# Optimization experiments

Hardware: AMD Instinct MI355X
Metric: run time of the kernel (lower is better)

The kernel has to match this reference:

```python
import jax, jax.numpy as jnp
import numpy as np

HID = 400
K = 10  # attention mixture components


def _lstm_cell(x, h, c, Wih, Whh, b):
    # torch gate order: i, f, g, o
    g = x @ Wih.T + h @ Whh.T + b
    i, f, gg, o = jnp.split(g, 4, axis=-1)
    c = jax.nn.sigmoid(f) * c + jax.nn.sigmoid(i) * jnp.tanh(gg)
    h = jax.nn.sigmoid(o) * jnp.tanh(c)
    return h, c


def setup_inputs() -> dict:
    key = jax.random.key(0)
    ks = jax.random.split(key, 14)
    B, T, U, D = 64, 600, 64, 60
    s = 0.08  # keep exp() in attention numerically tame
    strokes = jax.random.normal(ks[0], (B, T, 3), dtype=jnp.float32)
    ids = jax.random.randint(ks[1], (B, U), 0, D)
    onehots = jax.nn.one_hot(ids, D, dtype=jnp.float32)
    text_mask = jnp.ones((B, U), dtype=jnp.float32)
    W_ih1 = jax.random.normal(ks[2], (4 * HID, D + 3)) * s
    W_hh1 = jax.random.normal(ks[3], (4 * HID, HID)) * s
    b1 = jax.random.normal(ks[4], (4 * HID,)) * s  # b_ih + b_hh combined
    W_win = jax.random.normal(ks[5], (3 * K, HID)) * s
    b_win = jax.random.normal(ks[6], (3 * K,)) * s
    W_ih2 = jax.random.normal(ks[7], (4 * HID, 3 + D + HID)) * s
    W_hh2 = jax.random.normal(ks[8], (4 * HID, HID)) * s
    b2 = jax.random.normal(ks[9], (4 * HID,)) * s
    W_fc = jax.random.normal(ks[10], (121, 2 * HID)) * s
    b_fc = jax.random.normal(ks[11], (121,)) * s
    return {"strokes": strokes, "onehots": onehots, "text_mask": text_mask,
            "W_ih1": W_ih1, "W_hh1": W_hh1, "b1": b1,
            "W_win": W_win, "b_win": b_win,
            "W_ih2": W_ih2, "W_hh2": W_hh2, "b2": b2,
            "W_fc": W_fc, "b_fc": b_fc}


def reference(strokes, onehots, text_mask, W_ih1, W_hh1, b1, W_win, b_win,
              W_ih2, W_hh2, b2, W_fc, b_fc):
    B, T, _ = strokes.shape
    U = onehots.shape[1]
    u = jnp.arange(U, dtype=jnp.float32)

    def step1(carry, x_t):
        h0, c0, kappa, w = carry
        h0, c0 = _lstm_cell(jnp.concatenate([x_t, w], -1), h0, c0, W_ih1, W_hh1, b1)
        p = jnp.exp(h0 @ W_win.T + b_win)              # [B, 3K]
        alpha, beta, kap = jnp.split(p, 3, axis=-1)    # each [B, K]
        kappa = kappa + kap
        diff = kappa[:, None, :] - u[None, :, None]    # [B, U, K]
        phi = jnp.sum(alpha[:, None, :] * jnp.exp(-beta[:, None, :] * diff * diff), -1)
        phi = phi * text_mask                          # [B, U]
        w = jnp.einsum('bu,bud->bd', phi, onehots)     # [B, D]
        return (h0, c0, kappa, w), (h0, w, phi)

    z = jnp.zeros((B, HID), jnp.float32)
    init = (z, z, jnp.zeros((B, K), jnp.float32), onehots[:, 0, :])
    (h0f, c0f, kappa_f, w_f), (H1, Wt, Phi) = jax.lax.scan(step1, init, strokes.transpose(1, 0, 2))
    lstm1_out = H1.transpose(1, 0, 2)                  # [B, T, 400]
    attn_out = Wt.transpose(1, 0, 2)                   # [B, T, D]
    phi_last = Phi[-1]

    x2 = jnp.concatenate([strokes, attn_out, lstm1_out], -1)  # [B, T, 463]

    def step2(carry, x_t):
        h, c = carry
        h, c = _lstm_cell(x_t, h, c, W_ih2, W_hh2, b2)
        return (h, c), h

    (h1f, c1f), H2 = jax.lax.scan(step2, (z, z), x2.transpose(1, 0, 2))
    lstm2_out = H2.transpose(1, 0, 2)                  # [B, T, 400]

    out = jnp.concatenate([lstm1_out, lstm2_out], -1) @ W_fc.T + b_fc  # [B, T, 121]
    mu, log_sigma, pi, rho, eos = jnp.split(out, [40, 80, 100, 120], axis=-1)
    rho = jnp.tanh(rho)
    pi = jax.nn.softmax(pi, axis=-1)
    eos = jax.nn.sigmoid(-eos)
    mu = mu.reshape(B, T, 20, 2)
    sigma = log_sigma.reshape(B, T, 20, 2)  # original returns raw log-sigma reshaped
    return (pi, mu, sigma, rho, eos, w_f, kappa_f, phi_last, h0f, c0f, h1f, c1f)
```

## Files before the change

### kernel.cpp

```cpp
#include <hip/hip_runtime.h>
#include <hip/hip_bf16.h>
#include <math.h>

#define HIDN 400
#define KK   10
#define UU   64
#define DD   60
#define TT   600
#define FCIN 800
#define FCOUT 121

#define NH1  100
#define NH2  100
#define NWBK 32
#define WBAT 2
#define TOTB 232
#define THR  1024
#define NWAVE 16
#define CB   16
#define PSTR 68

#define SLOT1 25600
#define SLOTW 3840

#define PI_OFF    0
#define MU_OFF    768000
#define SIG_OFF   2304000
#define RHO_OFF   3840000
#define EOS_OFF   4608000
#define WF_OFF    4646400
#define KAPPA_OFF 4650240
#define PHI_OFF   4650880
#define H0F_OFF   4654976
#define C0F_OFF   4680576
#define H1F_OFF   4706176
#define C1F_OFF   4731776

#define WS_H1T   0
#define WS_H2T   15385600
#define WS_WHT   30771200
#define WS_XST   33079040
#define WS_WALL1 33194240
#define WS_WALL2 33935040
#define WS_WFCT  35315840
#define WS_CNT   35412640

#define CAI(i,g) ((((i)&7)*13+(g))*16)
#define CWI(i,g) (1664 + (((i)&7)*4+(g))*16)
#define CHI(i,g) (2176 + (((i)&7)*13+(g))*16)
#define CNT_INTS 3840

#define SMEM_F 32512

__device__ __forceinline__ float sigm(float x){ return 1.0f/(1.0f + expf(-x)); }
__device__ __forceinline__ int tgtn(int i, int n){ return n*((i>>3)+1); }

__device__ __forceinline__ void st_agent(float* p, float v){
  __hip_atomic_store(p, v, __ATOMIC_RELAXED, __HIP_MEMORY_SCOPE_AGENT);
}
__device__ __forceinline__ int ld_agent_i(const int* p){
  return __hip_atomic_load(p, __ATOMIC_RELAXED, __HIP_MEMORY_SCOPE_AGENT);
}
__device__ __forceinline__ void arrive(int* p){
  __hip_atomic_fetch_add(p, 1, __ATOMIC_RELAXED, __HIP_MEMORY_SCOPE_AGENT);
}
__device__ __forceinline__ void spin_ge(const int* w, int tgt){
  if (ld_agent_i(w) >= tgt) return;
  do { __builtin_amdgcn_s_sleep(1); } while (ld_agent_i(w) < tgt);
}

__global__ void prep_init(const float* __restrict__ onehots, const float* __restrict__ strokes,
                          float* __restrict__ H1t, float* __restrict__ H2t,
                          float* __restrict__ Wh,  float* __restrict__ XST,
                          int* __restrict__ cnts){
  int idx = blockIdx.x*blockDim.x + threadIdx.x;
  if (idx < SLOT1){ H1t[idx] = 0.f; H2t[idx] = 0.f; }
  if (idx < SLOTW){
    int d = idx >> 6, b = idx & 63;
    Wh[idx] = onehots[b*(UU*DD) + d];
  }
  if (idx < TT*3*64){
    int t = idx/192, rem = idx%192, comp = rem/64, b = rem%64;
    XST[idx] = strokes[(b*TT + t)*3 + comp];
  }
  if (idx < CNT_INTS) cnts[idx] = 0;
}

__global__ void prep_wall(const float* __restrict__ Wih1, const float* __restrict__ Whh1,
                          const float* __restrict__ Wih2, const float* __restrict__ Whh2,
                          float* __restrict__ WALL1, float* __restrict__ WALL2){
  int idx = blockIdx.x*blockDim.x + threadIdx.x;
  if (idx < 640000){
    int g = idx/400, k = idx%400;
    int q = g/400, j = g%400, pp = j>>2, c = 4*q + (j&3);
    WALL1[((size_t)pp*463 + k)*CB + c] = Whh1[idx];
  } else if (idx < 740800){
    int s = idx - 640000;
    int g = s/63, col = s%63;
    int q = g/400, j = g%400, pp = j>>2, c = 4*q + (j&3);
    int r = (col < 3) ? (460 + col) : (400 + col - 3);
    WALL1[((size_t)pp*463 + r)*CB + c] = Wih1[s];
  } else if (idx < 1380800){
    int s = idx - 740800;
    int g = s/400, k = s%400;
    int q = g/400, j = g%400, pp = j>>2, c = 4*q + (j&3);
    WALL2[((size_t)pp*863 + 400 + k)*CB + c] = Whh2[s];
  } else if (idx < 2121600){
    int s = idx - 1380800;
    int g = s/463, col = s%463;
    int q = g/400, j = g%400, pp = j>>2, c = 4*q + (j&3);
    int r = (col<3) ? (860+col) : (col<63 ? (800+col-3) : (col-63));
    WALL2[((size_t)pp*863 + r)*CB + c] = Wih2[s];
  }
}

__global__ void prep_wfc(const float* __restrict__ Wfc, float* __restrict__ WfcT){
  int idx = blockIdx.x*blockDim.x + threadIdx.x;
  if (idx >= FCIN*FCOUT) return;
  int k = idx / FCOUT, j = idx - k*FCOUT;
  WfcT[idx] = Wfc[j*FCIN + k];
}

__device__ __forceinline__ void gemv16(const float* __restrict__ x,
                                       const float* __restrict__ w,
                                       int n, int bg4, int cg4, float acc[16]){
  #pragma unroll 4
  for (int k=0;k<n;++k){
    const float4 xv = *(const float4*)(x + k*64 + bg4);
    const float4 wv = *(const float4*)(w + k*CB + cg4);
    acc[0]  = fmaf(wv.x, xv.x, acc[0]);
    acc[1]  = fmaf(wv.x, xv.y, acc[1]);
    acc[2]  = fmaf(wv.x, xv.z, acc[2]);
    acc[3]  = fmaf(wv.x, xv.w, acc[3]);
    acc[4]  = fmaf(wv.y, xv.x, acc[4]);
    acc[5]  = fmaf(wv.y, xv.y, acc[5]);
    acc[6]  = fmaf(wv.y, xv.z, acc[6]);
    acc[7]  = fmaf(wv.y, xv.w, acc[7]);
    acc[8]  = fmaf(wv.z, xv.x, acc[8]);
    acc[9]  = fmaf(wv.z, xv.y, acc[9]);
    acc[10] = fmaf(wv.z, xv.z, acc[10]);
    acc[11] = fmaf(wv.z, xv.w, acc[11]);
    acc[12] = fmaf(wv.w, xv.x, acc[12]);
    acc[13] = fmaf(wv.w, xv.y, acc[13]);
    acc[14] = fmaf(wv.w, xv.z, acc[14]);
    acc[15] = fmaf(wv.w, xv.w, acc[15]);
  }
}

__global__ __launch_bounds__(THR) void recurrent_kernel(
    const float* __restrict__ Wwin, const float* __restrict__ bwin,
    const float* __restrict__ b1g,  const float* __restrict__ b2g,
    const float* __restrict__ tmask,const float* __restrict__ onehots,
    const float* __restrict__ WALL1,const float* __restrict__ WALL2,
    float* __restrict__ H1t,        float* __restrict__ H2t,
    float* __restrict__ Wh,         const float* __restrict__ XST,
    int* __restrict__ cnts,         float* __restrict__ outp)
{
  const int p   = blockIdx.x;
  const int tid = threadIdx.x;
  __shared__ float SM[SMEM_F];

  if (p < NH1){
    const int wave = tid >> 6, lane = tid & 63;
    const int bg4  = (lane & 15) * 4;
    const int cg4  = (lane >> 4) * 4;
    float* WL1 = SM;          float* PART = SM + 7408;
    float* GRED= SM + 24816;  float* CS   = SM + 25840;
    float* BS  = SM + 26096;

    for (int idx = tid; idx < 463*CB; idx += THR) WL1[idx] = WALL1[(size_t)p*463*CB + idx];
    if (tid < 16){ int q = tid>>2, u = tid&3; BS[tid] = b1g[q*HIDN + 4*p + u]; }
    if (tid < 256) CS[tid] = 0.f;
    __syncthreads();

    for (int i = 0; i < TT; ++i){
      if (i >= 1){
        if (tid < 13) spin_ge(&cnts[CAI(i-1, tid)], tgtn(i-1, tid==12?4:8));
        asm volatile("" ::: "memory");
        __syncthreads();
      }
      float acc[16];
      #pragma unroll
      for (int z=0; z<16; ++z) acc[z] = 0.f;
      {
        const float* __restrict__ H1prev = H1t + (size_t)i*SLOT1;
        int k0 = wave*26, k1 = min(k0 + 26, 403);
        { int ka = k0, kb = min(k1, 400);
          if (kb > ka) gemv16(H1prev + ka*64, WL1 + ka*CB, kb-ka, bg4, cg4, acc); }
        { int ka = max(k0,400), kb = k1;
          if (kb > ka) gemv16(XST + i*192 + (ka-400)*64, WL1 + (460+(ka-400))*CB, kb-ka, bg4, cg4, acc); }
      }
      #pragma unroll
      for (int cc=0; cc<4; ++cc)
        *(float4*)&PART[(wave*16 + cg4 + cc)*PSTR + bg4] =
          make_float4(acc[cc*4+0], acc[cc*4+1], acc[cc*4+2], acc[cc*4+3]);
      __syncthreads();
      {
        int c = tid>>6, b = tid&63; float s = 0.f;
        #pragma unroll
        for (int w16=0; w16<NWAVE; ++w16) s += PART[(w16*16 + c)*PSTR + b];
        GRED[c*64 + b] = s;
      }
      __syncthreads();
      if (i >= 1){
        if (tid < 4) spin_ge(&cnts[CWI(i-1, tid)], tgtn(i-1, 8));
        asm volatile("" ::: "memory");
        __syncthreads();
      }
      if (tid < 256){
        int u = tid>>6, b = tid&63, j = 4*p + u;
        float gi = GRED[( 0+u)*64+b] + BS[ 0+u];
        float gf = GRED[( 4+u)*64+b] + BS[ 4+u];
        float gg = GRED[( 8+u)*64+b] + BS[ 8+u];
        float go = GRED[(12+u)*64+b] + BS[12+u];
        const float* __restrict__ Whp = Wh + (size_t)i*SLOTW + b;
        const float* __restrict__ Ww  = WL1 + 400*CB + u;
        #pragma unroll 4
        for (int d = 0; d < DD; ++d){
          float wv = Whp[d*64];
          gi = fmaf(wv, Ww[d*CB     ], gi);
          gf = fmaf(wv, Ww[d*CB +  4], gf);
          gg = fmaf(wv, Ww[d*CB +  8], gg);
          go = fmaf(wv, Ww[d*CB + 12], go);
        }
        float c_ = sigm(gf)*CS[u*64+b] + sigm(gi)*tanhf(gg);
        float h_ = sigm(go)*tanhf(c_);
        CS[u*64+b] = c_;
        st_agent(&H1t[(size_t)(i+1)*SLOT1 + j*64 + b], h_);
        if (i == TT-1){ outp[H0F_OFF + b*HIDN + j] = h_; outp[C0F_OFF + b*HIDN + j] = c_; }
      }
      __syncthreads();
      if (tid == 0) arrive(&cnts[CAI(i, p>>3)]);
    }
  } else if (p < NH1 + NH2){
    const int q2 = p - NH1;
    const int wave = tid >> 6, lane = tid & 63;
    const int bg4  = (lane & 15) * 4;
    const int cg4  = (lane >> 4) * 4;
    float* WL2 = SM;          float* PART = SM + 13808;
    float* GRED= SM + 31216;  float* CS   = SM + 32240;
    float* BS  = SM + 32496;

    for (int idx = tid; idx < 863*CB; idx += THR) WL2[idx] = WALL2[(size_t)q2*863*CB + idx];
    if (tid < 16){ int q = tid>>2, u = tid&3; BS[tid] = b2g[q*HIDN + 4*q2 + u]; }
    if (tid < 256) CS[tid] = 0.f;
    __syncthreads();

    for (int t2 = 0; t2 < TT; ++t2){
      if (tid < 13) spin_ge(&cnts[CAI(t2, tid)], tgtn(t2, tid==12?4:8));
      else if (tid >= 64 && tid < 68) spin_ge(&cnts[CWI(t2, tid-64)], tgtn(t2, 8));
      asm volatile("" ::: "memory");
      __syncthreads();
      float acc[16];
      #pragma unroll
      for (int z=0; z<16; ++z) acc[z] = 0.f;
      {
        const float* __restrict__ H1v = H1t + (size_t)(t2+1)*SLOT1;
        const float* __restrict__ Whv = Wh  + (size_t)(t2+1)*SLOTW;
        int k0 = wave*29, k1 = min(k0 + 29, 463);
        { int ka = k0, kb = min(k1, 400);
          if (kb > ka) gemv16(H1v + ka*64, WL2 + ka*CB, kb-ka, bg4, cg4, acc); }
        { int ka = max(k0,400), kb = min(k1, 460);
          if (kb > ka) gemv16(Whv + (ka-400)*64, WL2 + (800+(ka-400))*CB, kb-ka, bg4, cg4, acc); }
        { int ka = max(k0,460), kb = k1;
          if (kb > ka) gemv16(XST + t2*192 + (ka-460)*64, WL2 + (860+(ka-460))*CB, kb-ka, bg4, cg4, acc); }
      }
      if (t2 >= 1){
        if (tid < 13) spin_ge(&cnts[CHI(t2-1, tid)], tgtn(t2-1, tid==12?4:8));
        asm volatile("" ::: "memory");
        __syncthreads();
      }
      {
        const float* __restrict__ H2v = H2t + (size_t)t2*SLOT1;
        int k0 = wave*25, k1 = min(k0 + 25, 400);
        if (k1 > k0) gemv16(H2v + k0*64, WL2 + (400+k0)*CB, k1-k0, bg4, cg4, acc);
      }
      #pragma unroll
      for (int cc=0; cc<4; ++cc)
        *(float4*)&PART[(wave*16 + cg4 + cc)*PSTR + bg4] =
          make_float4(acc[cc*4+0], acc[cc*4+1], acc[cc*4+2], acc[cc*4+3]);
      __syncthreads();
      {
        int c = tid>>6, b = tid&63; float s = 0.f;
        #pragma unroll
        for (int w16=0; w16<NWAVE; ++w16) s += PART[(w16*16 + c)*PSTR + b];
        GRED[c*64 + b] = s;
      }
      __syncthreads();
      if (tid < 256){
        int u = tid>>6, b = tid&63, j = 4*q2 + u;
        float gi = GRED[( 0+u)*64+b] + BS[ 0+u];
        float gf = GRED[( 4+u)*64+b] + BS[ 4+u];
        float gg = GRED[( 8+u)*64+b] + BS[ 8+u];
        float go = GRED[(12+u)*64+b] + BS[12+u];
        float c_ = sigm(gf)*CS[u*64+b] + sigm(gi)*tanhf(gg);
        float h_ = sigm(go)*tanhf(c_);
        CS[u*64+b] = c_;
        st_agent(&H2t[(size_t)(t2+1)*SLOT1 + j*64 + b], h_);
        if (t2 == TT-1){ outp[H1F_OFF + b*HIDN + j] = h_; outp[C1F_OFF + b*HIDN + j] = c_; }
      }
      __syncthreads();
      if (tid == 0) arrive(&cnts[CHI(t2, q2>>3)]);
    }
  } else {
    const int wb = p - NH1 - NH2;
    const int b0 = wb * WBAT;
    float* WWT = SM;          float* ONE = SM + 13200;
    float* H1S = SM + 20880;  float* TMS = SM + 22080;
    float* PW  = SM + 22208;  float* KAP = SM + 22272;
    float* PHI = SM + 22304;

    for (int idx = tid; idx < 30*400; idx += THR){
      int j = idx/400, k = idx - j*400;
      WWT[k*33 + j] = Wwin[idx];
    }
    for (int idx = tid; idx < WBAT*UU*DD; idx += THR) ONE[idx] = onehots[b0*(UU*DD) + idx];
    if (tid < WBAT*UU) TMS[tid] = tmask[b0*UU + tid];
    if (tid < WBAT*16) KAP[tid] = 0.f;
    __syncthreads();

    for (int i = 0; i < TT; ++i){
      if (tid < 13) spin_ge(&cnts[CAI(i, tid)], tgtn(i, tid==12?4:8));
      asm volatile("" ::: "memory");
      __syncthreads();
      const float* __restrict__ H1now = H1t + (size_t)(i+1)*SLOT1;
      if (tid < 400){
        float2 v = *(const float2*)&H1now[tid*64 + b0];
        H1S[tid*3 + 0] = v.x;
        H1S[tid*3 + 1] = v.y;
      }
      __syncthreads();
      if (tid < 960){
        int ks = tid & 15, pair = tid >> 4;
        int b = pair / 30, j = pair - b*30;
        float s = 0.f;
        #pragma unroll
        for (int kk = 0; kk < 25; ++kk){
          int k = ks*25 + kk;
          s = fmaf(H1S[k*3 + b], WWT[k*33 + j], s);
        }
        s += __shfl_down(s, 8, 16);
        s += __shfl_down(s, 4, 16);
        s += __shfl_down(s, 2, 16);
        s += __shfl_down(s, 1, 16);
        if (ks == 0) PW[b*32 + j] = expf(s + bwin[j]);
      }
      __syncthreads();
      if (tid < WBAT*KK){
        int b = tid/KK, k = tid - b*KK;
        KAP[b*16 + k] += PW[b*32 + 20 + k];
      }
      __syncthreads();
      if (tid < WBAT*UU){
        int b = tid >> 6, u = tid & 63;
        float uf = (float)u, s = 0.f;
        #pragma unroll
        for (int q = 0; q < KK; ++q){
          float d = KAP[b*16 + q] - uf;
          s = fmaf(PW[b*32 + q], expf(-PW[b*32 + 10 + q]*d*d), s);
        }
        s *= TMS[b*64 + u];
        PHI[b*64 + u] = s;
        if (i == TT-1) outp[PHI_OFF + (b0+b)*UU + u] = s;
      }
      __syncthreads();
      if (tid < WBAT*DD){
        int b = tid/DD, d = tid - b*DD;
        float s = 0.f;
        #pragma unroll 8
        for (int u = 0; u < UU; ++u) s = fmaf(PHI[b*64 + u], ONE[b*(UU*DD) + u*DD + d], s);
        st_agent(&Wh[(size_t)(i+1)*SLOTW + d*64 + b0 + b], s);
        if (i == TT-1) outp[WF_OFF + (b0+b)*DD + d] = s;
      }
      if (i == TT-1 && tid < WBAT*KK){
        int b = tid/KK, k = tid - b*KK;
        outp[KAPPA_OFF + (b0+b)*KK + k] = KAP[b*16 + k];
      }
      __syncthreads();
      if (tid == 0) arrive(&cnts[CWI(i, wb>>3)]);
    }
  }
}

__global__ __launch_bounds__(128) void fc2_kernel(
    const float* __restrict__ H1t, const float* __restrict__ H2t,
    const float* __restrict__ WfcT, const float* __restrict__ bfc,
    float* __restrict__ outp)
{
  const int t   = blockIdx.x;
  const int tid = threadIdx.x;
  __shared__ float Xs[8][64];
  __shared__ float OUT[FCOUT][65];
  float acc[64];
  #pragma unroll
  for (int b=0;b<64;++b) acc[b]=0.f;
  const float* __restrict__ base1 = H1t + (size_t)(t+1)*SLOT1;
  const float* __restrict__ base2 = H2t + (size_t)(t+1)*SLOT1;

  for (int kb=0; kb<100; ++kb){
    __syncthreads();
    #pragma unroll
    for (int e=0;e<4;++e){
      int idx = e*128 + tid;
      int row = idx>>6, b = idx&63;
      int k = kb*8 + row;
      Xs[row][b] = (k<400) ? base1[k*64+b] : base2[(k-400)*64+b];
    }
    __syncthreads();
    if (tid < FCOUT){
      #pragma unroll
      for (int kk=0;kk<8;++kk){
        float wv = WfcT[(kb*8+kk)*FCOUT + tid];
        #pragma unroll
        for (int b4=0;b4<16;++b4){
          float4 xv = *(const float4*)&Xs[kk][b4*4];
          acc[b4*4+0] = fmaf(wv, xv.x, acc[b4*4+0]);
          acc[b4*4+1] = fmaf(wv, xv.y, acc[b4*4+1]);
          acc[b4*4+2] = fmaf(wv, xv.z, acc[b4*4+2]);
          acc[b4*4+3] = fmaf(wv, xv.w, acc[b4*4+3]);
        }
      }
    }
  }
  if (tid < FCOUT){
    float bj = bfc[tid];
    #pragma unroll
    for (int b=0;b<64;++b) OUT[tid][b] = acc[b] + bj;
  }
  __syncthreads();
  if (tid < 64){
    const int b = tid;
    const size_t pos = (size_t)b*TT + t;
    for (int j=0;j<40;++j) outp[MU_OFF  + pos*40 + j] = OUT[j][b];
    for (int j=0;j<40;++j) outp[SIG_OFF + pos*40 + j] = OUT[40+j][b];
    float m = -1e30f;
    for (int q=0;q<20;++q) m = fmaxf(m, OUT[80+q][b]);
    float e[20], s=0.f;
    for (int q=0;q<20;++q){ e[q]=expf(OUT[80+q][b]-m); s+=e[q]; }
    float inv = 1.f/s;
    for (int q=0;q<20;++q) outp[PI_OFF  + pos*20 + q] = e[q]*inv;
    for (int q=0;q<20;++q) outp[RHO_OFF + pos*20 + q] = tanhf(OUT[100+q][b]);
    outp[EOS_OFF + pos] = 1.0f/(1.0f + expf(OUT[120][b]));
  }
}

extern "C" void kernel_launch(void* const* d_in, const int* in_sizes, int n_in,
                              void* d_out, int out_size, void* d_ws, size_t ws_size,
                              hipStream_t stream){
  (void)in_sizes; (void)n_in; (void)out_size; (void)ws_size;
  const float* strokes = (const float*)d_in[0];
  const float* onehots = (const float*)d_in[1];
  const float* tmask   = (const float*)d_in[2];
  const float* Wih1    = (const float*)d_in[3];
  const float* Whh1    = (const float*)d_in[4];
  const float* b1      = (const float*)d_in[5];
  const float* Wwin    = (const float*)d_in[6];
  const float* bwin    = (const float*)d_in[7];
  const float* Wih2    = (const float*)d_in[8];
  const float* Whh2    = (const float*)d_in[9];
  const float* b2      = (const float*)d_in[10];
  const float* Wfc     = (const float*)d_in[11];
  const float* bfc     = (const float*)d_in[12];

  float* ws    = (float*)d_ws;
  float* outp  = (float*)d_out;
  float* H1t   = ws + WS_H1T;
  float* H2t   = ws + WS_H2T;
  float* Wh    = ws + WS_WHT;
  float* XST   = ws + WS_XST;
  float* WALL1 = ws + WS_WALL1;
  float* WALL2 = ws + WS_WALL2;
  float* WfcT  = ws + WS_WFCT;
  int*   cnts  = (int*)(ws + WS_CNT);

  hipLaunchKernelGGL(prep_init, dim3((TT*3*64 + 255)/256), dim3(256), 0, stream,
                     onehots, strokes, H1t, H2t, Wh, XST, cnts);
  hipLaunchKernelGGL(prep_wall, dim3((2121600 + 255)/256), dim3(256), 0, stream,
                     Wih1, Whh1, Wih2, Whh2, WALL1, WALL2);
  hipLaunchKernelGGL(prep_wfc, dim3((FCIN*FCOUT + 255)/256), dim3(256), 0, stream,
                     Wfc, WfcT);

  hipLaunchKernelGGL(recurrent_kernel, dim3(TOTB), dim3(THR), 0, stream,
                     Wwin, bwin, b1, b2, tmask, onehots, WALL1, WALL2,
                     H1t, H2t, Wh, XST, cnts, outp);

  hipLaunchKernelGGL(fc2_kernel, dim3(TT), dim3(128), 0, stream,
                     H1t, H2t, WfcT, bfc, outp);
}
```

Before: 6.567 ms.

## Split LSTM1 batch into two interleaved halves to overlap with attention blocks

The layer-1 recurrent blocks now process the 64-sample batch as two 32-sample groups in alternating half-steps, each with its own per-group counters. Attention blocks are split by group and wait only on their own half. While one half waits on its attention result, the other half's GEMV can proceed, which is meant to hide the serial dependency chain between LSTM1 and the attention window. The cost is twice as many barriers and spin-waits per timestep, plus narrower GEMV tiles.

```diff
diff --git a/kernel.cpp b/kernel.cpp
--- a/kernel.cpp
+++ b/kernel.cpp
@@ -19,6 +19,7 @@
 #define NWAVE 16
 #define CB   16
 #define PSTR 68
+#define PSTR2 36
 
 #define SLOT1 25600
 #define SLOTW 3840
@@ -45,10 +46,10 @@
 #define WS_WFCT  35315840
 #define WS_CNT   35412640
 
-#define CAI(i,g) ((((i)&7)*13+(g))*16)
-#define CWI(i,g) (1664 + (((i)&7)*4+(g))*16)
-#define CHI(i,g) (2176 + (((i)&7)*13+(g))*16)
-#define CNT_INTS 3840
+#define CAI(grp,i,g) ((((grp)*8 + ((i)&7))*13 + (g))*16)
+#define CWI(grp,i,g) (3328 + (((grp)*8 + ((i)&7))*2 + (g))*16)
+#define CHI(i,g)     (3840 + (((i)&7)*13 + (g))*16)
+#define CNT_INTS 5504
 
 #define SMEM_F 32512
 
@@ -146,6 +147,23 @@
     acc[15] = fmaf(wv.w, xv.w, acc[15]);
   }
 }
+__device__ __forceinline__ void gemv8(const float* __restrict__ x,
+                                      const float* __restrict__ w,
+                                      int n, int bg4, int cg2, float acc[8]){
+  #pragma unroll 4
+  for (int k=0;k<n;++k){
+    const float4 xv = *(const float4*)(x + k*64 + bg4);
+    const float2 wv = *(const float2*)(w + k*CB + cg2);
+    acc[0] = fmaf(wv.x, xv.x, acc[0]);
+    acc[1] = fmaf(wv.x, xv.y, acc[1]);
+    acc[2] = fmaf(wv.x, xv.z, acc[2]);
+    acc[3] = fmaf(wv.x, xv.w, acc[3]);
+    acc[4] = fmaf(wv.y, xv.x, acc[4]);
+    acc[5] = fmaf(wv.y, xv.y, acc[5]);
+    acc[6] = fmaf(wv.y, xv.z, acc[6]);
+    acc[7] = fmaf(wv.y, xv.w, acc[7]);
+  }
+}
 
 __global__ __launch_bounds__(THR) void recurrent_kernel(
     const float* __restrict__ Wwin, const float* __restrict__ bwin,
@@ -162,58 +180,56 @@
 
   if (p < NH1){
     const int wave = tid >> 6, lane = tid & 63;
-    const int bg4  = (lane & 15) * 4;
-    const int cg4  = (lane >> 4) * 4;
+    const int bg4  = (lane & 7) * 4;
+    const int cg2  = (lane >> 3) * 2;
     float* WL1 = SM;          float* PART = SM + 7408;
-    float* GRED= SM + 24816;  float* CS   = SM + 25840;
-    float* BS  = SM + 26096;
+    float* GRED= SM + 16624;  float* CS   = SM + 17136;
+    float* BS  = SM + 17392;
 
     for (int idx = tid; idx < 463*CB; idx += THR) WL1[idx] = WALL1[(size_t)p*463*CB + idx];
     if (tid < 16){ int q = tid>>2, u = tid&3; BS[tid] = b1g[q*HIDN + 4*p + u]; }
     if (tid < 256) CS[tid] = 0.f;
     __syncthreads();
 
-    for (int i = 0; i < TT; ++i){
+    for (int j = 0; j < 2*TT; ++j){
+      const int grp = j & 1, i = j >> 1;
+      const int gb  = grp * 32;
       if (i >= 1){
-        if (tid < 13) spin_ge(&cnts[CAI(i-1, tid)], tgtn(i-1, tid==12?4:8));
+        if (tid < 13) spin_ge(&cnts[CAI(grp, i-1, tid)], tgtn(i-1, tid==12?4:8));
         asm volatile("" ::: "memory");
         __syncthreads();
       }
-      float acc[16];
-      #pragma unroll
-      for (int z=0; z<16; ++z) acc[z] = 0.f;
+      float acc[8] = {0,0,0,0,0,0,0,0};
       {
-        const float* __restrict__ H1prev = H1t + (size_t)i*SLOT1;
+        const float* __restrict__ H1prev = H1t + (size_t)i*SLOT1 + gb;
         int k0 = wave*26, k1 = min(k0 + 26, 403);
         { int ka = k0, kb = min(k1, 400);
-          if (kb > ka) gemv16(H1prev + ka*64, WL1 + ka*CB, kb-ka, bg4, cg4, acc); }
+          if (kb > ka) gemv8(H1prev + ka*64, WL1 + ka*CB, kb-ka, bg4, cg2, acc); }
         { int ka = max(k0,400), kb = k1;
-          if (kb > ka) gemv16(XST + i*192 + (ka-400)*64, WL1 + (460+(ka-400))*CB, kb-ka, bg4, cg4, acc); }
-      }
-      #pragma unroll
-      for (int cc=0; cc<4; ++cc)
-        *(float4*)&PART[(wave*16 + cg4 + cc)*PSTR + bg4] =
-          make_float4(acc[cc*4+0], acc[cc*4+1], acc[cc*4+2], acc[cc*4+3]);
-      __syncthreads();
-      {
-        int c = tid>>6, b = tid&63; float s = 0.f;
+          if (kb > ka) gemv8(XST + i*192 + (ka-400)*64 + gb, WL1 + (460+(ka-400))*CB, kb-ka, bg4, cg2, acc); }
+      }
+      *(float4*)&PART[(wave*16 + cg2  )*PSTR2 + bg4] = make_float4(acc[0],acc[1],acc[2],acc[3]);
+      *(float4*)&PART[(wave*16 + cg2+1)*PSTR2 + bg4] = make_float4(acc[4],acc[5],acc[6],acc[7]);
+      __syncthreads();
+      if (tid < 512){
+        int c = tid>>5, b = tid&31; float s = 0.f;
         #pragma unroll
-        for (int w16=0; w16<NWAVE; ++w16) s += PART[(w16*16 + c)*PSTR + b];
-        GRED[c*64 + b] = s;
+        for (int w16=0; w16<NWAVE; ++w16) s += PART[(w16*16 + c)*PSTR2 + b];
+        GRED[c*32 + b] = s;
       }
       __syncthreads();
       if (i >= 1){
-        if (tid < 4) spin_ge(&cnts[CWI(i-1, tid)], tgtn(i-1, 8));
+        if (tid < 2) spin_ge(&cnts[CWI(grp, i-1, tid)], tgtn(i-1, 8));
         asm volatile("" ::: "memory");
         __syncthreads();
       }
-      if (tid < 256){
-        int u = tid>>6, b = tid&63, j = 4*p + u;
-        float gi = GRED[( 0+u)*64+b] + BS[ 0+u];
-        float gf = GRED[( 4+u)*64+b] + BS[ 4+u];
-        float gg = GRED[( 8+u)*64+b] + BS[ 8+u];
-        float go = GRED[(12+u)*64+b] + BS[12+u];
-        const float* __restrict__ Whp = Wh + (size_t)i*SLOTW + b;
+      if (tid < 128){
+        int u = tid>>5, b = tid&31, jj = 4*p + u;
+        float gi = GRED[( 0+u)*32+b] + BS[ 0+u];
+        float gf = GRED[( 4+u)*32+b] + BS[ 4+u];
+        float gg = GRED[( 8+u)*32+b] + BS[ 8+u];
+        float go = GRED[(12+u)*32+b] + BS[12+u];
+        const float* __restrict__ Whp = Wh + (size_t)i*SLOTW + gb + b;
         const float* __restrict__ Ww  = WL1 + 400*CB + u;
         #pragma unroll 4
         for (int d = 0; d < DD; ++d){
@@ -223,14 +239,15 @@
           gg = fmaf(wv, Ww[d*CB +  8], gg);
           go = fmaf(wv, Ww[d*CB + 12], go);
         }
-        float c_ = sigm(gf)*CS[u*64+b] + sigm(gi)*tanhf(gg);
+        float* cs = &CS[grp*128 + u*32 + b];
+        float c_ = sigm(gf)*(*cs) + sigm(gi)*tanhf(gg);
         float h_ = sigm(go)*tanhf(c_);
-        CS[u*64+b] = c_;
-        st_agent(&H1t[(size_t)(i+1)*SLOT1 + j*64 + b], h_);
-        if (i == TT-1){ outp[H0F_OFF + b*HIDN + j] = h_; outp[C0F_OFF + b*HIDN + j] = c_; }
-      }
-      __syncthreads();
-      if (tid == 0) arrive(&cnts[CAI(i, p>>3)]);
+        *cs = c_;
+        st_agent(&H1t[(size_t)(i+1)*SLOT1 + jj*64 + gb + b], h_);
+        if (i == TT-1){ outp[H0F_OFF + (gb+b)*HIDN + jj] = h_; outp[C0F_OFF + (gb+b)*HIDN + jj] = c_; }
+      }
+      __syncthreads();
+      if (tid == 0) arrive(&cnts[CAI(grp, i, p>>3)]);
     }
   } else if (p < NH1 + NH2){
     const int q2 = p - NH1;
@@ -247,8 +264,10 @@
     __syncthreads();
 
     for (int t2 = 0; t2 < TT; ++t2){
-      if (tid < 13) spin_ge(&cnts[CAI(t2, tid)], tgtn(t2, tid==12?4:8));
-      else if (tid >= 64 && tid < 68) spin_ge(&cnts[CWI(t2, tid-64)], tgtn(t2, 8));
+      if (tid < 13)                      spin_ge(&cnts[CAI(0, t2, tid)],    tgtn(t2, tid==12?4:8));
+      else if (tid >= 64 && tid < 77)    spin_ge(&cnts[CAI(1, t2, tid-64)], tgtn(t2, (tid-64)==12?4:8));
+      else if (tid >= 128 && tid < 132){ int g=(tid-128)>>1, l=(tid-128)&1;
+                                         spin_ge(&cnts[CWI(g, t2, l)],      tgtn(t2, 8)); }
       asm volatile("" ::: "memory");
       __syncthreads();
       float acc[16];
@@ -288,7 +307,7 @@
       }
       __syncthreads();
       if (tid < 256){
-        int u = tid>>6, b = tid&63, j = 4*q2 + u;
+        int u = tid>>6, b = tid&63, jj = 4*q2 + u;
         float gi = GRED[( 0+u)*64+b] + BS[ 0+u];
         float gf = GRED[( 4+u)*64+b] + BS[ 4+u];
         float gg = GRED[( 8+u)*64+b] + BS[ 8+u];
@@ -296,8 +315,8 @@
         float c_ = sigm(gf)*CS[u*64+b] + sigm(gi)*tanhf(gg);
         float h_ = sigm(go)*tanhf(c_);
         CS[u*64+b] = c_;
-        st_agent(&H2t[(size_t)(t2+1)*SLOT1 + j*64 + b], h_);
-        if (t2 == TT-1){ outp[H1F_OFF + b*HIDN + j] = h_; outp[C1F_OFF + b*HIDN + j] = c_; }
+        st_agent(&H2t[(size_t)(t2+1)*SLOT1 + jj*64 + b], h_);
+        if (t2 == TT-1){ outp[H1F_OFF + b*HIDN + jj] = h_; outp[C1F_OFF + b*HIDN + jj] = c_; }
       }
       __syncthreads();
       if (tid == 0) arrive(&cnts[CHI(t2, q2>>3)]);
@@ -305,14 +324,15 @@
   } else {
     const int wb = p - NH1 - NH2;
     const int b0 = wb * WBAT;
+    const int grp = wb >> 4;
     float* WWT = SM;          float* ONE = SM + 13200;
     float* H1S = SM + 20880;  float* TMS = SM + 22080;
     float* PW  = SM + 22208;  float* KAP = SM + 22272;
     float* PHI = SM + 22304;
 
     for (int idx = tid; idx < 30*400; idx += THR){
-      int j = idx/400, k = idx - j*400;
-      WWT[k*33 + j] = Wwin[idx];
+      int jj = idx/400, k = idx - jj*400;
+      WWT[k*33 + jj] = Wwin[idx];
     }
     for (int idx = tid; idx < WBAT*UU*DD; idx += THR) ONE[idx] = onehots[b0*(UU*DD) + idx];
     if (tid < WBAT*UU) TMS[tid] = tmask[b0*UU + tid];
@@ -320,7 +340,7 @@
     __syncthreads();
 
     for (int i = 0; i < TT; ++i){
-      if (tid < 13) spin_ge(&cnts[CAI(i, tid)], tgtn(i, tid==12?4:8));
+      if (tid < 13) spin_ge(&cnts[CAI(grp, i, tid)], tgtn(i, tid==12?4:8));
       asm volatile("" ::: "memory");
       __syncthreads();
       const float* __restrict__ H1now = H1t + (size_t)(i+1)*SLOT1;
@@ -332,18 +352,18 @@
       __syncthreads();
       if (tid < 960){
         int ks = tid & 15, pair = tid >> 4;
-        int b = pair / 30, j = pair - b*30;
+        int b = pair / 30, jj = pair - b*30;
         float s = 0.f;
         #pragma unroll
         for (int kk = 0; kk < 25; ++kk){
           int k = ks*25 + kk;
-          s = fmaf(H1S[k*3 + b], WWT[k*33 + j], s);
+          s = fmaf(H1S[k*3 + b], WWT[k*33 + jj], s);
         }
         s += __shfl_down(s, 8, 16);
         s += __shfl_down(s, 4, 16);
         s += __shfl_down(s, 2, 16);
         s += __shfl_down(s, 1, 16);
-        if (ks == 0) PW[b*32 + j] = expf(s + bwin[j]);
+        if (ks == 0) PW[b*32 + jj] = expf(s + bwin[jj]);
       }
       __syncthreads();
       if (tid < WBAT*KK){
@@ -377,7 +397,7 @@
         outp[KAPPA_OFF + (b0+b)*KK + k] = KAP[b*16 + k];
       }
       __syncthreads();
-      if (tid == 0) arrive(&cnts[CWI(i, wb>>3)]);
+      if (tid == 0) arrive(&cnts[CWI(grp, i, (wb & 15) >> 3)]);
     }
   }
 }
```

Result: slower. 9.356 ms (+42.5%).

## Let each window wave wait on its own chunk counter and read H1 directly

Applied to the files above, without the earlier changes.

In the attention-window blocks, each of 13 waves now spins only on the counter for its own 32-row slice of h1. It then computes its partial dot products straight from global memory, with no block-wide barrier and no staging of H1 into shared memory. Partial sums go to a shared buffer and are reduced by one wave before the exp. This removes two __syncthreads per timestep and lets waves start as soon as their chunk is ready. The trade-off is uncoalesced, repeated global loads of H1 values across lanes.

```diff
diff --git a/kernel.cpp b/kernel.cpp
--- a/kernel.cpp
+++ b/kernel.cpp
@@ -305,10 +305,14 @@
   } else {
     const int wb = p - NH1 - NH2;
     const int b0 = wb * WBAT;
-    float* WWT = SM;          float* ONE = SM + 13200;
-    float* H1S = SM + 20880;  float* TMS = SM + 22080;
-    float* PW  = SM + 22208;  float* KAP = SM + 22272;
-    float* PHI = SM + 22304;
+    const int wave = tid >> 6, lane = tid & 63;
+    float* WWT  = SM;
+    float* ONE  = SM + 13200;
+    float* PARTW= SM + 20880;
+    float* TMS  = SM + 21712;
+    float* PW   = SM + 21840;
+    float* KAP  = SM + 21904;
+    float* PHI  = SM + 21936;
 
     for (int idx = tid; idx < 30*400; idx += THR){
       int j = idx/400, k = idx - j*400;
@@ -320,30 +324,39 @@
     __syncthreads();
 
     for (int i = 0; i < TT; ++i){
-      if (tid < 13) spin_ge(&cnts[CAI(i, tid)], tgtn(i, tid==12?4:8));
-      asm volatile("" ::: "memory");
-      __syncthreads();
       const float* __restrict__ H1now = H1t + (size_t)(i+1)*SLOT1;
-      if (tid < 400){
-        float2 v = *(const float2*)&H1now[tid*64 + b0];
-        H1S[tid*3 + 0] = v.x;
-        H1S[tid*3 + 1] = v.y;
-      }
-      __syncthreads();
-      if (tid < 960){
-        int ks = tid & 15, pair = tid >> 4;
-        int b = pair / 30, j = pair - b*30;
+      if (wave < 13){
+        if (lane == 0) spin_ge(&cnts[CAI(i, wave)], tgtn(i, wave==12?4:8));
+        asm volatile("" ::: "memory");
+        const int base = wave*32;
+        const int b = lane >> 5, jj = lane & 31;
         float s = 0.f;
-        #pragma unroll
-        for (int kk = 0; kk < 25; ++kk){
-          int k = ks*25 + kk;
-          s = fmaf(H1S[k*3 + b], WWT[k*33 + j], s);
+        if (jj < 30){
+          if (wave == 12){
+            #pragma unroll
+            for (int kk = 0; kk < 16; ++kk){
+              int k = base + kk;
+              s = fmaf(H1now[k*64 + b0 + b], WWT[k*33 + jj], s);
+            }
+          } else {
+            #pragma unroll
+            for (int kk = 0; kk < 32; ++kk){
+              int k = base + kk;
+              s = fmaf(H1now[k*64 + b0 + b], WWT[k*33 + jj], s);
+            }
+          }
         }
-        s += __shfl_down(s, 8, 16);
-        s += __shfl_down(s, 4, 16);
-        s += __shfl_down(s, 2, 16);
-        s += __shfl_down(s, 1, 16);
-        if (ks == 0) PW[b*32 + j] = expf(s + bwin[j]);
+        PARTW[wave*64 + lane] = s;
+      }
+      __syncthreads();
+      if (tid < 64){
+        int b = tid >> 5, jj = tid & 31;
+        if (jj < 30){
+          float s = 0.f;
+          #pragma unroll
+          for (int g = 0; g < 13; ++g) s += PARTW[g*64 + tid];
+          PW[b*32 + jj] = expf(s + bwin[jj]);
+        }
       }
       __syncthreads();
       if (tid < WBAT*KK){
```

Result: slower. 8.872 ms (+35.1%).
